# Optimization experiments

Measured on AMD Instinct MI355X. Metric: run time of the kernel, lower is better.

## Reference

```python
import jax, jax.numpy as jnp
import numpy as np

HEAD_SIZE = 64
EMBED_DIM = 1024
N_HEAD = EMBED_DIM // HEAD_SIZE
BATCH, SEQ = 8, 2048


def wkv6(r, k, v, w, u, s):
    # r,k,v,w: (B,T,H,D); u: (H,D); s: (B,H,D,D) indexed state[j,i] (j: key dim, i: value dim)
    decay = jnp.exp(-jnp.exp(w))  # RWKV-6 CUDA kernel computes exp(-exp(w)) per channel/step

    def step(state, inp):
        r_t, k_t, v_t, d_t = inp  # each (B,H,D)
        kv = k_t[..., :, None] * v_t[..., None, :]  # (B,H,D,D)
        y_t = jnp.einsum('bhj,bhji->bhi', r_t, state + u[..., :, None] * kv)
        state = d_t[..., :, None] * state + kv
        return state, y_t

    xs = tuple(jnp.moveaxis(t, 1, 0) for t in (r, k, v, decay))  # time-major (T,B,H,D)
    s_final, y = jax.lax.scan(step, s, xs)
    return jnp.moveaxis(y, 0, 1), s_final  # (B,T,H,D), (B,H,D,D)


def setup_inputs() -> dict:
    key = jax.random.key(0)
    ks = jax.random.split(key, 20)
    C, H, D = EMBED_DIM, N_HEAD, HEAD_SIZE
    f = jnp.float32
    inp = {
        'x': jax.random.normal(ks[0], (BATCH, SEQ, C), f),
        'x_last': jax.random.normal(ks[1], (BATCH, SEQ, C), f),
        's': jnp.zeros((BATCH, H, D, D), f),
        'miu_x': jax.random.uniform(ks[2], (1, 1, C), f),
        'lambda_': jax.random.uniform(ks[3], (5, 1, 1, C), f),
        'A': jax.random.normal(ks[4], (C, 160), f) * 0.01,
        'B_lora': jax.random.normal(ks[5], (5, 32, C), f) * 0.01,
        'time_decay_miu': jax.random.uniform(ks[6], (1, 1, C), f, minval=-6.0, maxval=-0.5),
        'td_A': jax.random.normal(ks[7], (C, 64), f) * 0.01,
        'td_B': jax.random.normal(ks[8], (64, C), f) * 0.01,
        'u': jax.random.normal(ks[9], (H, D), f) * 0.5,
        'W_k': jax.random.normal(ks[10], (C, C), f) * (0.05 / C ** 0.5),
        'W_v': jax.random.normal(ks[11], (C, C), f) * (0.5 / C ** 0.5),
        'W_r': jax.random.normal(ks[12], (C, C), f) * (0.5 / C ** 0.5),
        'W_o': jax.random.normal(ks[13], (C, C), f) * (0.5 / C ** 0.5),
        'W_g1': jax.random.normal(ks[14], (C, 160), f) * 0.01,
        'W_g2': jax.random.normal(ks[15], (160, C), f) * 0.01,
        'gn_gamma': jnp.ones((C,), f),
        'gn_beta': jnp.zeros((C,), f),
    }
    return inp


def reference(x, x_last, s, miu_x, lambda_, A, B_lora, time_decay_miu, td_A, td_B, u,
              W_k, W_v, W_r, W_o, W_g1, W_g2, gn_gamma, gn_beta):
    Bsz, T, C = x.shape
    H, D = C // HEAD_SIZE, HEAD_SIZE
    x_raw = x
    # ddlerp: token-shift mix with data-dependent mus from batched LoRA
    b_a = x_last - x
    xl = x + b_a * miu_x
    # NB: source uses a raw .view(5, B*T, 32) (no transpose) -- replicate exactly with reshape
    t1 = jnp.tanh(xl @ A).reshape(5, Bsz * T, 32)
    miu = lambda_ + jnp.einsum('fmk,fkc->fmc', t1, B_lora).reshape(5, Bsz, T, C)
    xdd = x[None] + b_a[None] * miu  # (5,B,T,C)
    w0, k0, v0, r0, g0 = xdd[0], xdd[1], xdd[2], xdd[3], xdd[4]
    # decay LoRA
    w = time_decay_miu + jnp.tanh(w0 @ td_A) @ td_B  # (B,T,C)
    k = (k0 @ W_k.T) * jnp.exp(jnp.minimum(w, 0.0))
    v = v0 @ W_v.T
    r = r0 @ W_r.T
    g = jnp.tanh(g0 @ W_g1) @ W_g2
    rh, kh, vh, wh = (t.reshape(Bsz, T, H, D) for t in (r, k, v, w))
    y, s_new = wkv6(rh, kh, vh, wh, u, s)
    # GroupNorm over (B*T, n_head groups of head_size), eps = 1e-5 * n_head
    y = y.reshape(Bsz * T, H, D)
    eps = 1e-5 * H
    mu = y.mean(axis=-1, keepdims=True)
    var = y.var(axis=-1, keepdims=True)
    yn = (y - mu) / jnp.sqrt(var + eps)
    yn = yn * gn_gamma.reshape(H, D) + gn_beta.reshape(H, D)
    yn = yn.reshape(Bsz, T, C)
    out = (yn * g) @ W_o.T
    return out, x_raw, s_new
```

## Files before the change

### kernel.cpp

```cpp
#include <hip/hip_runtime.h>
#include <hip/hip_bf16.h>

namespace {

typedef __attribute__((ext_vector_type(8))) short short8x;
typedef __attribute__((ext_vector_type(4))) float f32x4;

__device__ __forceinline__ float bf2f(unsigned short h) {
    return __uint_as_float(((unsigned int)h) << 16);
}
__device__ __forceinline__ unsigned short f2bf(float f) {
    __hip_bfloat16 h = __float2bfloat16(f);
    return *reinterpret_cast<unsigned short*>(&h);
}

enum { ACT_NONE = 0, ACT_TANH = 1 };
enum { EPI_NONE = 0, EPI_KSCALE = 1, EPI_ADDVEC = 2 };

template <int ACT, int EPI, int SBF>
__launch_bounds__(256) __global__
void gemm_mfma(int Npad, int K, int Nreal, int Cstride,
               const unsigned short* __restrict__ A,
               const unsigned short* __restrict__ B,
               float* __restrict__ Cf, unsigned short* __restrict__ Cb,
               const float* __restrict__ epi)
{
    __shared__ unsigned short as_[128 * 32];
    __shared__ unsigned short bs_[128 * 32];
    const int tid = threadIdx.x;
    const int lane = tid & 63;
    const int wave = tid >> 6;
    const int m0 = blockIdx.y << 7;
    const int n0 = blockIdx.x << 7;
    const int wm = (wave >> 1) << 6;
    const int wn = (wave & 1) << 6;

    f32x4 acc[4][4];
    const f32x4 zero = {0.f, 0.f, 0.f, 0.f};
#pragma unroll
    for (int i = 0; i < 4; ++i)
#pragma unroll
        for (int j = 0; j < 4; ++j) acc[i][j] = zero;

    const int sr = tid >> 2;
    const int sc4 = tid & 3;

    for (int k0 = 0; k0 < K; k0 += 32) {
        const uint4 a0 = *(const uint4*)(A + (size_t)(m0 + sr) * K + k0 + sc4 * 8);
        const uint4 a1 = *(const uint4*)(A + (size_t)(m0 + 64 + sr) * K + k0 + sc4 * 8);
        const uint4 b0 = *(const uint4*)(B + (size_t)(n0 + sr) * K + k0 + sc4 * 8);
        const uint4 b1 = *(const uint4*)(B + (size_t)(n0 + 64 + sr) * K + k0 + sc4 * 8);
        __syncthreads();
        {
            int r = sr, p = sc4 ^ ((r >> 1) & 3);
            *(uint4*)&as_[r * 32 + p * 8] = a0;
            *(uint4*)&bs_[r * 32 + p * 8] = b0;
            r = 64 + sr; p = sc4 ^ ((r >> 1) & 3);
            *(uint4*)&as_[r * 32 + p * 8] = a1;
            *(uint4*)&bs_[r * 32 + p * 8] = b1;
        }
        __syncthreads();
        const int q = lane >> 4;
        const int l15 = lane & 15;
        short8x af[4], bfr[4];
#pragma unroll
        for (int i = 0; i < 4; ++i) {
            const int m = wm + (i << 4) + l15;
            const int pa = q ^ ((m >> 1) & 3);
            af[i] = *(const short8x*)&as_[m * 32 + pa * 8];
            const int n = wn + (i << 4) + l15;
            const int pb = q ^ ((n >> 1) & 3);
            bfr[i] = *(const short8x*)&bs_[n * 32 + pb * 8];
        }
#pragma unroll
        for (int i = 0; i < 4; ++i)
#pragma unroll
            for (int j = 0; j < 4; ++j)
                acc[i][j] = __builtin_amdgcn_mfma_f32_16x16x32_bf16(af[i], bfr[j], acc[i][j], 0, 0, 0);
    }

    const int q = lane >> 4;
    const int cn = lane & 15;
#pragma unroll
    for (int i = 0; i < 4; ++i) {
#pragma unroll
        for (int j = 0; j < 4; ++j) {
#pragma unroll
            for (int rr = 0; rr < 4; ++rr) {
                const int row = m0 + wm + (i << 4) + (q << 2) + rr;
                const int col = n0 + wn + (j << 4) + cn;
                if (col >= Nreal) continue;
                float v = acc[i][j][rr];
                if constexpr (ACT == ACT_TANH) v = tanhf(v);
                if constexpr (EPI == EPI_KSCALE)
                    v *= __expf(fminf(epi[(size_t)row * 1024 + col], 0.f));
                if constexpr (EPI == EPI_ADDVEC) v += epi[col];
                if constexpr (SBF) Cb[(size_t)row * Cstride + col] = f2bf(v);
                else               Cf[(size_t)row * Cstride + col] = v;
            }
        }
    }
}

__launch_bounds__(256) __global__
void mix_k(const float* __restrict__ x, const float* __restrict__ xla,
           const float* __restrict__ mux, unsigned short* __restrict__ out)
{
    const size_t idx = ((size_t)blockIdx.x * 256 + threadIdx.x) * 4;
    const int c = (int)(idx & 1023);
    const float4 xv = *(const float4*)(x + idx);
    const float4 xl = *(const float4*)(xla + idx);
    const float4 mu = *(const float4*)(mux + c);
    ushort4 o;
    o.x = f2bf(xv.x + (xl.x - xv.x) * mu.x);
    o.y = f2bf(xv.y + (xl.y - xv.y) * mu.y);
    o.z = f2bf(xv.z + (xl.z - xv.z) * mu.z);
    o.w = f2bf(xv.w + (xl.w - xv.w) * mu.w);
    *(ushort4*)(out + idx) = o;
}

__launch_bounds__(256) __global__
void convert_k(const float* __restrict__ src, unsigned short* __restrict__ dst)
{
    const size_t idx = ((size_t)blockIdx.x * 256 + threadIdx.x) * 4;
    const float4 v = *(const float4*)(src + idx);
    ushort4 o;
    o.x = f2bf(v.x); o.y = f2bf(v.y); o.z = f2bf(v.z); o.w = f2bf(v.w);
    *(ushort4*)(dst + idx) = o;
}

__launch_bounds__(256) __global__
void transpose_k(const float* __restrict__ src, unsigned short* __restrict__ dst,
                 int K, int Nsrc)
{
    const int k = blockIdx.x * 256 + threadIdx.x;
    const int n = blockIdx.y;
    if (k < K)
        dst[(size_t)n * K + k] = (n < Nsrc) ? f2bf(src[(size_t)k * Nsrc + n]) : (unsigned short)0;
}

__launch_bounds__(256) __global__
void xdd_k(const float* __restrict__ x, const float* __restrict__ xla,
           const unsigned short* __restrict__ t1, const float* __restrict__ blora,
           const float* __restrict__ lam, unsigned short* __restrict__ out, int f)
{
    __shared__ float sh[4][32];
    const int tid = threadIdx.x;
    const int m0 = blockIdx.x << 2;
    if (tid < 128) {
        const int r = tid >> 5, kk = tid & 31;
        sh[r][kk] = bf2f(t1[(size_t)f * 524288 + (size_t)(m0 + r) * 32 + kk]);
    }
    __syncthreads();
    const int c0 = tid << 2;
    const float* bl = blora + f * 32768 + c0;
    float dot[4][4];
#pragma unroll
    for (int r = 0; r < 4; ++r)
#pragma unroll
        for (int j = 0; j < 4; ++j) dot[r][j] = 0.f;
    for (int kk = 0; kk < 32; ++kk) {
        const float4 b4 = *(const float4*)(bl + (size_t)kk * 1024);
#pragma unroll
        for (int r = 0; r < 4; ++r) {
            const float tv = sh[r][kk];
            dot[r][0] = fmaf(tv, b4.x, dot[r][0]);
            dot[r][1] = fmaf(tv, b4.y, dot[r][1]);
            dot[r][2] = fmaf(tv, b4.z, dot[r][2]);
            dot[r][3] = fmaf(tv, b4.w, dot[r][3]);
        }
    }
    const float4 l4 = *(const float4*)(lam + f * 1024 + c0);
#pragma unroll
    for (int r = 0; r < 4; ++r) {
        const size_t idx = (size_t)(m0 + r) * 1024 + c0;
        const float4 xv = *(const float4*)(x + idx);
        const float4 xl = *(const float4*)(xla + idx);
        ushort4 o;
        o.x = f2bf(xv.x + (xl.x - xv.x) * (l4.x + dot[r][0]));
        o.y = f2bf(xv.y + (xl.y - xv.y) * (l4.y + dot[r][1]));
        o.z = f2bf(xv.z + (xl.z - xv.z) * (l4.z + dot[r][2]));
        o.w = f2bf(xv.w + (xl.w - xv.w) * (l4.w + dot[r][3]));
        *(ushort4*)(out + idx) = o;
    }
}

__launch_bounds__(256) __global__
void zero_k(float4* __restrict__ p)
{
    const float4 z = {0.f, 0.f, 0.f, 0.f};
    p[(size_t)blockIdx.x * 256 + threadIdx.x] = z;
}

__launch_bounds__(256) __global__
void decay_k(float* __restrict__ p)
{
    const size_t idx = ((size_t)blockIdx.x * 256 + threadIdx.x) * 4;
    const float4 v = *(const float4*)(p + idx);
    float4 o;
    o.x = __expf(-__expf(v.x));
    o.y = __expf(-__expf(v.y));
    o.z = __expf(-__expf(v.z));
    o.w = __expf(-__expf(v.w));
    *(float4*)(p + idx) = o;
}

#define BF_LO(x) __uint_as_float((x) << 16)
#define BF_HI(x) __uint_as_float((x) & 0xFFFF0000u)

#define WKV_LOAD(RV, KV, DV, VVv, T0)                                         \
    do {                                                                      \
        _Pragma("unroll")                                                     \
        for (int tt = 0; tt < 4; ++tt) {                                      \
            const size_t o_ = (size_t)((T0) + tt) * 1024;                     \
            RV[tt] = *(const uint4*)(rp + o_);                                \
            KV[tt] = *(const uint4*)(kp + o_);                                \
            DV[tt][0] = *(const float4*)(dp + o_);                            \
            DV[tt][1] = *(const float4*)(dp + o_ + 4);                        \
            VVv[tt] = vp[o_];                                                 \
        }                                                                     \
    } while (0)

#define WKV_PROC(RV, KV, DV, VVv, T0)                                         \
    do {                                                                      \
        _Pragma("unroll")                                                     \
        for (int tt = 0; tt < 4; ++tt) {                                      \
            const float vi_ = bf2f(VVv[tt]);                                  \
            float rj[8], kj[8], dj[8];                                        \
            rj[0] = BF_LO(RV[tt].x); rj[1] = BF_HI(RV[tt].x);                 \
            rj[2] = BF_LO(RV[tt].y); rj[3] = BF_HI(RV[tt].y);                 \
            rj[4] = BF_LO(RV[tt].z); rj[5] = BF_HI(RV[tt].z);                 \
            rj[6] = BF_LO(RV[tt].w); rj[7] = BF_HI(RV[tt].w);                 \
            kj[0] = BF_LO(KV[tt].x); kj[1] = BF_HI(KV[tt].x);                 \
            kj[2] = BF_LO(KV[tt].y); kj[3] = BF_HI(KV[tt].y);                 \
            kj[4] = BF_LO(KV[tt].z); kj[5] = BF_HI(KV[tt].z);                 \
            kj[6] = BF_LO(KV[tt].w); kj[7] = BF_HI(KV[tt].w);                 \
            dj[0] = DV[tt][0].x; dj[1] = DV[tt][0].y;                         \
            dj[2] = DV[tt][0].z; dj[3] = DV[tt][0].w;                         \
            dj[4] = DV[tt][1].x; dj[5] = DV[tt][1].y;                         \
            dj[6] = DV[tt][1].z; dj[7] = DV[tt][1].w;                         \
            float ya0_ = 0.f, ya1_ = 0.f;                                     \
            _Pragma("unroll")                                                 \
            for (int jj = 0; jj < 8; ++jj) {                                  \
                const float t_ = kj[jj] * vi_;                                \
                const float a_ = fmaf(u8[jj], t_, s[jj]);                     \
                if (jj & 1) ya1_ = fmaf(rj[jj], a_, ya1_);                    \
                else        ya0_ = fmaf(rj[jj], a_, ya0_);                    \
                s[jj] = fmaf(dj[jj], s[jj], t_);                              \
            }                                                                 \
            unsafeAtomicAdd(yp + (size_t)((T0) + tt) * 1024, ya0_ + ya1_);    \
        }                                                                     \
    } while (0)

#define P1_LOAD(KV, DV, VVv, T0)                                              \
    do {                                                                      \
        _Pragma("unroll")                                                     \
        for (int tt = 0; tt < 4; ++tt) {                                      \
            const size_t o_ = (size_t)((T0) + tt) * 1024;                     \
            KV[tt] = *(const uint4*)(kp + o_);                                \
            DV[tt][0] = *(const float4*)(dp + o_);                            \
            DV[tt][1] = *(const float4*)(dp + o_ + 4);                        \
            VVv[tt] = vp[o_];                                                 \
        }                                                                     \
    } while (0)

#define P1_PROC(KV, DV, VVv)                                                  \
    do {                                                                      \
        _Pragma("unroll")                                                     \
        for (int tt = 0; tt < 4; ++tt) {                                      \
            const float vi_ = bf2f(VVv[tt]);                                  \
            float kj[8], dj[8];                                               \
            kj[0] = BF_LO(KV[tt].x); kj[1] = BF_HI(KV[tt].x);                 \
            kj[2] = BF_LO(KV[tt].y); kj[3] = BF_HI(KV[tt].y);                 \
            kj[4] = BF_LO(KV[tt].z); kj[5] = BF_HI(KV[tt].z);                 \
            kj[6] = BF_LO(KV[tt].w); kj[7] = BF_HI(KV[tt].w);                 \
            dj[0] = DV[tt][0].x; dj[1] = DV[tt][0].y;                         \
            dj[2] = DV[tt][0].z; dj[3] = DV[tt][0].w;                         \
            dj[4] = DV[tt][1].x; dj[5] = DV[tt][1].y;                         \
            dj[6] = DV[tt][1].z; dj[7] = DV[tt][1].w;                         \
            _Pragma("unroll")                                                 \
            for (int jj = 0; jj < 8; ++jj) {                                  \
                const float t_ = kj[jj] * vi_;                                \
                s[jj] = fmaf(dj[jj], s[jj], t_);                              \
                D[jj] *= dj[jj];                                              \
            }                                                                 \
        }                                                                     \
    } while (0)

__launch_bounds__(64) __global__
void wkv_p1(const unsigned short* __restrict__ k, const unsigned short* __restrict__ v,
            const float* __restrict__ d,
            float* __restrict__ slocal, float* __restrict__ dprod)
{
    const int blk = blockIdx.x;
    const int bh = blk & 127;
    const int jc = (blk >> 7) & 7;
    const int tc = blk >> 10;
    const int h = bh & 15;
    const int l = threadIdx.x;
    const int jbase = jc << 3;

    float s[8], D[8];
#pragma unroll
    for (int jj = 0; jj < 8; ++jj) { s[jj] = 0.f; D[jj] = 1.f; }

    const size_t base = (size_t)(bh >> 4) * (2048 * 1024) + (size_t)tc * 131072 + (h << 6);
    const unsigned short* kp = k + base + jbase;
    const float*          dp = d + base + jbase;
    const unsigned short* vp = v + base + l;

    uint4 kA[4]; float4 dA[4][2]; unsigned short vA[4];
    uint4 kB[4]; float4 dB[4][2]; unsigned short vB[4];

    P1_LOAD(kA, dA, vA, 0);
    for (int c = 0; c < 32; c += 2) {
        P1_LOAD(kB, dB, vB, (c + 1) * 4);
        P1_PROC(kA, dA, vA);
        if (c + 2 < 32) P1_LOAD(kA, dA, vA, (c + 2) * 4);
        P1_PROC(kB, dB, vB);
    }
    const size_t cb = (size_t)(tc * 128 + bh) * 64 + jbase;
#pragma unroll
    for (int jj = 0; jj < 8; ++jj) slocal[(cb + jj) * 64 + l] = s[jj];
    if (l == 0) {
#pragma unroll
        for (int jj = 0; jj < 8; ++jj) dprod[cb + jj] = D[jj];
    }
}

__launch_bounds__(64) __global__
void wkv_p2(const float* __restrict__ s_in, const float* __restrict__ slocal,
            const float* __restrict__ dprod, float* __restrict__ sstart,
            float* __restrict__ s_out)
{
    const int blk = blockIdx.x;
    const int bh = blk & 127;
    const int jc = blk >> 7;
    const int l = threadIdx.x;
    const int jbase = jc << 3;

    float s[8];
    const size_t sb = (size_t)bh * 4096;
#pragma unroll
    for (int jj = 0; jj < 8; ++jj) s[jj] = s_in[sb + (size_t)(jbase + jj) * 64 + l];

    for (int c = 0; c < 16; ++c) {
        const size_t cb = (size_t)(c * 128 + bh) * 64 + jbase;
#pragma unroll
        for (int jj = 0; jj < 8; ++jj) sstart[(cb + jj) * 64 + l] = s[jj];
#pragma unroll
        for (int jj = 0; jj < 8; ++jj)
            s[jj] = fmaf(dprod[cb + jj], s[jj], slocal[(cb + jj) * 64 + l]);
    }
#pragma unroll
    for (int jj = 0; jj < 8; ++jj) s_out[sb + (size_t)(jbase + jj) * 64 + l] = s[jj];
}

__launch_bounds__(64) __global__
void wkv_p3(const unsigned short* __restrict__ r, const unsigned short* __restrict__ k,
            const unsigned short* __restrict__ v, const float* __restrict__ d,
            const float* __restrict__ u, const float* __restrict__ sstart,
            float* __restrict__ y)
{
    const int blk = blockIdx.x;
    const int bh = blk & 127;
    const int jc = (blk >> 7) & 7;
    const int tc = blk >> 10;
    const int h = bh & 15;
    const int l = threadIdx.x;
    const int jbase = jc << 3;

    float s[8];
    const size_t cb = (size_t)(tc * 128 + bh) * 64 + jbase;
#pragma unroll
    for (int jj = 0; jj < 8; ++jj) s[jj] = sstart[(cb + jj) * 64 + l];

    float u8[8];
#pragma unroll
    for (int jj = 0; jj < 8; ++jj) u8[jj] = u[(h << 6) + jbase + jj];

    const size_t base = (size_t)(bh >> 4) * (2048 * 1024) + (size_t)tc * 131072 + (h << 6);
    const unsigned short* rp = r + base + jbase;
    const unsigned short* kp = k + base + jbase;
    const float*          dp = d + base + jbase;
    const unsigned short* vp = v + base + l;
    float*                yp = y + base + l;

    uint4 rA[4], kA[4]; float4 dA[4][2]; unsigned short vA[4];
    uint4 rB[4], kB[4]; float4 dB[4][2]; unsigned short vB[4];

    WKV_LOAD(rA, kA, dA, vA, 0);
    for (int c = 0; c < 32; c += 2) {
        WKV_LOAD(rB, kB, dB, vB, (c + 1) * 4);
        WKV_PROC(rA, kA, dA, vA, c * 4);
        if (c + 2 < 32) WKV_LOAD(rA, kA, dA, vA, (c + 2) * 4);
        WKV_PROC(rB, kB, dB, vB, (c + 1) * 4);
    }
}

__launch_bounds__(256) __global__
void gn_k(const float* __restrict__ y0,
          const unsigned short* __restrict__ g, const float* __restrict__ gam,
          const float* __restrict__ bet, unsigned short* __restrict__ z)
{
    const int tid = threadIdx.x;
    const size_t row = blockIdx.x;
    const int c0 = tid << 2;
    const size_t idx = row * 1024 + c0;
    const float4 a = *(const float4*)(y0 + idx);
    const float yv0 = a.x, yv1 = a.y, yv2 = a.z, yv3 = a.w;
    float sm = yv0 + yv1 + yv2 + yv3;
    float q = yv0 * yv0 + yv1 * yv1 + yv2 * yv2 + yv3 * yv3;
#pragma unroll
    for (int off = 1; off < 16; off <<= 1) {
        sm += __shfl_xor(sm, off, 64);
        q += __shfl_xor(q, off, 64);
    }
    const float mean = sm * (1.f / 64.f);
    const float var = q * (1.f / 64.f) - mean * mean;
    const float rstd = rsqrtf(var + 1.6e-4f);
    const float4 gm = *(const float4*)(gam + c0);
    const float4 bt = *(const float4*)(bet + c0);
    const ushort4 gg = *(const ushort4*)(g + idx);
    ushort4 o;
    o.x = f2bf(((yv0 - mean) * rstd * gm.x + bt.x) * bf2f(gg.x));
    o.y = f2bf(((yv1 - mean) * rstd * gm.y + bt.y) * bf2f(gg.y));
    o.z = f2bf(((yv2 - mean) * rstd * gm.z + bt.z) * bf2f(gg.z));
    o.w = f2bf(((yv3 - mean) * rstd * gm.w + bt.w) * bf2f(gg.w));
    *(ushort4*)(z + idx) = o;
}

__launch_bounds__(256) __global__
void copy_k(const float4* __restrict__ src, float4* __restrict__ dst)
{
    const size_t i = (size_t)blockIdx.x * 256 + threadIdx.x;
    dst[i] = src[i];
}

}

extern "C" void kernel_launch(void* const* d_in, const int* in_sizes, int n_in,
                              void* d_out, int out_size, void* d_ws, size_t ws_size,
                              hipStream_t stream)
{
    (void)in_sizes; (void)n_in; (void)out_size; (void)ws_size;
    const float* x     = (const float*)d_in[0];
    const float* xla   = (const float*)d_in[1];
    const float* s_in  = (const float*)d_in[2];
    const float* mux   = (const float*)d_in[3];
    const float* lam   = (const float*)d_in[4];
    const float* Amat  = (const float*)d_in[5];
    const float* blora = (const float*)d_in[6];
    const float* tdmu  = (const float*)d_in[7];
    const float* tdA   = (const float*)d_in[8];
    const float* tdB   = (const float*)d_in[9];
    const float* u     = (const float*)d_in[10];
    const float* Wk    = (const float*)d_in[11];
    const float* Wv    = (const float*)d_in[12];
    const float* Wr    = (const float*)d_in[13];
    const float* Wo    = (const float*)d_in[14];
    const float* Wg1   = (const float*)d_in[15];
    const float* Wg2   = (const float*)d_in[16];
    const float* gam   = (const float*)d_in[17];
    const float* bet   = (const float*)d_in[18];

    float* out  = (float*)d_out;
    float* xraw = out + 16777216;
    float* snew = out + 2 * 16777216;

    char* ws = (char*)d_ws;
    unsigned short* mixb   = (unsigned short*)(ws);
    unsigned short* xddb   = (unsigned short*)(ws + 33554432);
    unsigned short* t1     = (unsigned short*)(ws + 67108864);
    unsigned short* tanh64 = (unsigned short*)(ws + 72351744);
    unsigned short* tanhg  = (unsigned short*)(ws + 74448896);
    unsigned short* kbuf   = (unsigned short*)(ws + 79691776);
    unsigned short* vbuf   = (unsigned short*)(ws + 113246208);
    unsigned short* rbuf   = (unsigned short*)(ws + 146800640);
    unsigned short* gbuf   = (unsigned short*)(ws + 180355072);
    unsigned short* wkt    = (unsigned short*)(ws + 213909504);
    unsigned short* wvt    = (unsigned short*)(ws + 216006656);
    unsigned short* wrt    = (unsigned short*)(ws + 218103808);
    unsigned short* wot    = (unsigned short*)(ws + 220200960);
    unsigned short* at_    = (unsigned short*)(ws + 222298112);
    unsigned short* tdat   = (unsigned short*)(ws + 222822400);
    unsigned short* tdbt   = (unsigned short*)(ws + 223084544);
    unsigned short* wg1t   = (unsigned short*)(ws + 223215616);
    unsigned short* wg2t   = (unsigned short*)(ws + 223739904);

    float* w  = out;
    float* y0 = xraw;
    float* slocal = (float*)ws;
    float* sstart = (float*)(ws + 33554432);
    float* dprod  = (float*)(ws + 67108864);

    convert_k<<<1024, 256, 0, stream>>>(Wk, wkt);
    convert_k<<<1024, 256, 0, stream>>>(Wv, wvt);
    convert_k<<<1024, 256, 0, stream>>>(Wr, wrt);
    convert_k<<<1024, 256, 0, stream>>>(Wo, wot);
    transpose_k<<<dim3(4, 256), 256, 0, stream>>>(Amat, at_, 1024, 160);
    transpose_k<<<dim3(4, 128), 256, 0, stream>>>(tdA, tdat, 1024, 64);
    transpose_k<<<dim3(1, 1024), 256, 0, stream>>>(tdB, tdbt, 64, 1024);
    transpose_k<<<dim3(4, 256), 256, 0, stream>>>(Wg1, wg1t, 1024, 160);
    transpose_k<<<dim3(1, 1024), 256, 0, stream>>>(Wg2, wg2t, 160, 1024);

    mix_k<<<16384, 256, 0, stream>>>(x, xla, mux, mixb);
    gemm_mfma<ACT_TANH, EPI_NONE, 1><<<dim3(2, 128), 256, 0, stream>>>(
        256, 1024, 160, 160, mixb, at_, nullptr, t1, nullptr);

    xdd_k<<<4096, 256, 0, stream>>>(x, xla, t1, blora, lam, xddb, 0);
    gemm_mfma<ACT_TANH, EPI_NONE, 1><<<dim3(1, 128), 256, 0, stream>>>(
        128, 1024, 64, 64, xddb, tdat, nullptr, tanh64, nullptr);
    gemm_mfma<ACT_NONE, EPI_ADDVEC, 0><<<dim3(8, 128), 256, 0, stream>>>(
        1024, 64, 1024, 1024, tanh64, tdbt, w, nullptr, tdmu);

    xdd_k<<<4096, 256, 0, stream>>>(x, xla, t1, blora, lam, xddb, 1);
    gemm_mfma<ACT_NONE, EPI_KSCALE, 1><<<dim3(8, 128), 256, 0, stream>>>(
        1024, 1024, 1024, 1024, xddb, wkt, nullptr, kbuf, w);

    decay_k<<<16384, 256, 0, stream>>>(w);

    xdd_k<<<4096, 256, 0, stream>>>(x, xla, t1, blora, lam, xddb, 2);
    gemm_mfma<ACT_NONE, EPI_NONE, 1><<<dim3(8, 128), 256, 0, stream>>>(
        1024, 1024, 1024, 1024, xddb, wvt, nullptr, vbuf, nullptr);

    xdd_k<<<4096, 256, 0, stream>>>(x, xla, t1, blora, lam, xddb, 3);
    gemm_mfma<ACT_NONE, EPI_NONE, 1><<<dim3(8, 128), 256, 0, stream>>>(
        1024, 1024, 1024, 1024, xddb, wrt, nullptr, rbuf, nullptr);

    xdd_k<<<4096, 256, 0, stream>>>(x, xla, t1, blora, lam, xddb, 4);
    gemm_mfma<ACT_TANH, EPI_NONE, 1><<<dim3(2, 128), 256, 0, stream>>>(
        256, 1024, 160, 160, xddb, wg1t, nullptr, tanhg, nullptr);
    gemm_mfma<ACT_NONE, EPI_NONE, 1><<<dim3(8, 128), 256, 0, stream>>>(
        1024, 160, 1024, 1024, tanhg, wg2t, nullptr, gbuf, nullptr);

    zero_k<<<16384, 256, 0, stream>>>((float4*)y0);
    wkv_p1<<<16384, 64, 0, stream>>>(kbuf, vbuf, w, slocal, dprod);
    wkv_p2<<<1024, 64, 0, stream>>>(s_in, slocal, dprod, sstart, snew);
    wkv_p3<<<16384, 64, 0, stream>>>(rbuf, kbuf, vbuf, w, u, sstart, y0);

    gn_k<<<16384, 256, 0, stream>>>(y0, gbuf, gam, bet, kbuf);

    gemm_mfma<ACT_NONE, EPI_NONE, 0><<<dim3(8, 128), 256, 0, stream>>>(
        1024, 1024, 1024, 1024, kbuf, wot, out, nullptr, nullptr);

    copy_k<<<16384, 256, 0, stream>>>((const float4*)x, (float4*)xraw);
}
```

Measured before the change: 1.676 ms.

## Replace atomic y accumulation in wkv_p3 with shared-memory block reduction

wkv_p3 now runs one 512-thread block per (chunk, batch-head), with each of its 8 wavefronts covering one 8-wide slice of the key dimension. Partial outputs go to shared memory and are summed by four wavefronts, which store y directly instead of using atomic adds. This removes the global float atomics and the separate zero-fill kernel. In exchange it adds a block-wide barrier every 4 timesteps, uses fewer and larger blocks, and double-buffers the reduction slots to avoid a second barrier.

```diff
diff --git a/kernel.cpp b/kernel.cpp
--- a/kernel.cpp
+++ b/kernel.cpp
@@ -186,13 +186,6 @@
 }
 
 __launch_bounds__(256) __global__
-void zero_k(float4* __restrict__ p)
-{
-    const float4 z = {0.f, 0.f, 0.f, 0.f};
-    p[(size_t)blockIdx.x * 256 + threadIdx.x] = z;
-}
-
-__launch_bounds__(256) __global__
 void decay_k(float* __restrict__ p)
 {
     const size_t idx = ((size_t)blockIdx.x * 256 + threadIdx.x) * 4;
@@ -221,7 +214,7 @@
         }                                                                     \
     } while (0)
 
-#define WKV_PROC(RV, KV, DV, VVv, T0)                                         \
+#define P3_PROC(RV, KV, DV, VVv, SLOT, T0)                                    \
     do {                                                                      \
         _Pragma("unroll")                                                     \
         for (int tt = 0; tt < 4; ++tt) {                                      \
@@ -248,7 +241,14 @@
                 else        ya0_ = fmaf(rj[jj], a_, ya0_);                    \
                 s[jj] = fmaf(dj[jj], s[jj], t_);                              \
             }                                                                 \
-            unsafeAtomicAdd(yp + (size_t)((T0) + tt) * 1024, ya0_ + ya1_);    \
+            red[SLOT][w][tt][l] = ya0_ + ya1_;                                \
+        }                                                                     \
+        __syncthreads();                                                      \
+        if (w < 4) {                                                          \
+            float acc_ = red[SLOT][0][w][l];                                  \
+            _Pragma("unroll")                                                 \
+            for (int w_ = 1; w_ < 8; ++w_) acc_ += red[SLOT][w_][w][l];       \
+            yp[(size_t)((T0) + w) * 1024] = acc_;                             \
         }                                                                     \
     } while (0)
 
@@ -356,7 +356,7 @@
     for (int jj = 0; jj < 8; ++jj) s_out[sb + (size_t)(jbase + jj) * 64 + l] = s[jj];
 }
 
-__launch_bounds__(64) __global__
+__launch_bounds__(512) __global__
 void wkv_p3(const unsigned short* __restrict__ r, const unsigned short* __restrict__ k,
             const unsigned short* __restrict__ v, const float* __restrict__ d,
             const float* __restrict__ u, const float* __restrict__ sstart,
@@ -364,11 +364,14 @@
 {
     const int blk = blockIdx.x;
     const int bh = blk & 127;
-    const int jc = (blk >> 7) & 7;
-    const int tc = blk >> 10;
+    const int tc = blk >> 7;
     const int h = bh & 15;
-    const int l = threadIdx.x;
-    const int jbase = jc << 3;
+    const int tid = threadIdx.x;
+    const int w = tid >> 6;
+    const int l = tid & 63;
+    const int jbase = w << 3;
+
+    __shared__ float red[2][8][4][64];
 
     float s[8];
     const size_t cb = (size_t)(tc * 128 + bh) * 64 + jbase;
@@ -392,9 +395,9 @@
     WKV_LOAD(rA, kA, dA, vA, 0);
     for (int c = 0; c < 32; c += 2) {
         WKV_LOAD(rB, kB, dB, vB, (c + 1) * 4);
-        WKV_PROC(rA, kA, dA, vA, c * 4);
+        P3_PROC(rA, kA, dA, vA, 0, c * 4);
         if (c + 2 < 32) WKV_LOAD(rA, kA, dA, vA, (c + 2) * 4);
-        WKV_PROC(rB, kB, dB, vB, (c + 1) * 4);
+        P3_PROC(rB, kB, dB, vB, 1, (c + 1) * 4);
     }
 }
 
@@ -534,10 +537,9 @@
     gemm_mfma<ACT_NONE, EPI_NONE, 1><<<dim3(8, 128), 256, 0, stream>>>(
         1024, 160, 1024, 1024, tanhg, wg2t, nullptr, gbuf, nullptr);
 
-    zero_k<<<16384, 256, 0, stream>>>((float4*)y0);
     wkv_p1<<<16384, 64, 0, stream>>>(kbuf, vbuf, w, slocal, dprod);
     wkv_p2<<<1024, 64, 0, stream>>>(s_in, slocal, dprod, sstart, snew);
-    wkv_p3<<<16384, 64, 0, stream>>>(rbuf, kbuf, vbuf, w, u, sstart, y0);
+    wkv_p3<<<2048, 512, 0, stream>>>(rbuf, kbuf, vbuf, w, u, sstart, y0);
 
     gn_k<<<16384, 256, 0, stream>>>(y0, gbuf, gam, bet, kbuf);
 
```

Measured after the change: 1.602 ms. 1.05x faster.
